# Kernel tuning notes

Hardware: AMD Instinct MI355X
Metric: run time of the kernel (lower is better)

The kernel has to match this reference:

```python
import jax, jax.numpy as jnp
import numpy as np

SEQ, D = 4096, 1024  # vector_size == dimension == 1024


def setup_inputs() -> dict:
    key = jax.random.key(0)
    ks = jax.random.split(key, 7)
    s = 1.0 / np.sqrt(D)
    return {
        "X": jax.random.normal(ks[0], (SEQ, D), dtype=jnp.float32),
        "Wq": jax.random.normal(ks[1], (D, D), dtype=jnp.float32) * s,
        "bq": jax.random.normal(ks[2], (D,), dtype=jnp.float32) * s,
        "Wk": jax.random.normal(ks[3], (D, D), dtype=jnp.float32) * s,
        "bk": jax.random.normal(ks[4], (D,), dtype=jnp.float32) * s,
        "Wv": jax.random.normal(ks[5], (D, D), dtype=jnp.float32) * s,
        "bv": jax.random.normal(ks[6], (D,), dtype=jnp.float32) * s,
    }


def reference(X, Wq, bq, Wk, bk, Wv, bv):
    # Batched QKV projections (nn.Linear: x @ W^T + b), replacing the per-vector loop.
    Q = X @ Wq.T + bq            # [S, D]
    K = X @ Wk.T + bk            # [S, D]
    V = X @ Wv.T + bv            # [S, D]
    scale = 1.0 / jnp.sqrt(jnp.asarray(D, dtype=X.dtype))
    scores = (Q @ K.T) * scale   # [S, S]
    attn = jax.nn.softmax(scores, axis=1)
    return attn @ V              # [S, D]
```

## Files before the change

kernel.cpp:

```cpp
#include <hip/hip_runtime.h>
#include <hip/hip_bf16.h>
#include <stdint.h>


typedef __bf16 bf16_t;
typedef __bf16 bf16x4 __attribute__((ext_vector_type(4)));
typedef __bf16 bf16x8 __attribute__((ext_vector_type(8)));
typedef float f32x4 __attribute__((ext_vector_type(4)));

#define AS1 __attribute__((address_space(1)))
#define AS3 __attribute__((address_space(3)))

__device__ __forceinline__ void async_ld16(const void* g, void* l) {
  __builtin_amdgcn_global_load_lds((AS1 void*)g, (AS3 void*)l, 16, 0, 0);
}

#define SBAR() __builtin_amdgcn_sched_barrier(0)
#define BARRIER()                 \
  do {                            \
    SBAR();                       \
    __builtin_amdgcn_s_barrier(); \
    SBAR();                       \
  } while (0)
#define LGKM0()                                         \
  do {                                                  \
    asm volatile("s_waitcnt lgkmcnt(0)" ::: "memory");  \
    SBAR();                                             \
  } while (0)

template <int MODE>
__global__ __launch_bounds__(512, 2) void gemm8(
    const bf16_t* __restrict__ A, const bf16_t* __restrict__ B, const int ld,
    const int Klen, bf16_t* __restrict__ o0, bf16_t* __restrict__ o1,
    bf16_t* __restrict__ o2, const float* __restrict__ b0,
    const float* __restrict__ b1, const float* __restrict__ b2,
    float* __restrict__ fout, float* __restrict__ rowsum) {
  extern __shared__ bf16_t smem[];

  const int t = threadIdx.x;
  const int lane = t & 63;
  const int wave = t >> 6;
  const int wm = wave >> 2;
  const int wn = wave & 3;
  const int q = lane >> 4;
  const int l16 = lane & 15;
  const int xf = l16 & 7;

  int m0, n0, k0 = 0, zz = 0;
  const int bid = blockIdx.x;
  if constexpr (MODE == 0) {
    const int x = bid & 7, sl = bid >> 3;
    m0 = ((x >> 1) * 4 + (sl & 3)) * 256;
    n0 = ((x & 1) * 6 + (sl >> 2)) * 256;
  } else if constexpr (MODE == 1) {
    const int x = bid & 7, sl = bid >> 3;
    m0 = ((x >> 2) * 8 + (sl >> 2)) * 256;
    n0 = ((x & 3) * 4 + (sl & 3)) * 256;
  } else {
    const int x = bid & 7, sl = bid >> 3;
    zz = x >> 1;
    m0 = ((x & 1) * 8 + (sl >> 2)) * 256;
    n0 = (sl & 3) * 256;
    k0 = zz * Klen;
  }

  const int srow = t >> 3;
  const int c8s = ((t & 7) ^ (srow & 7)) * 8;
  const bf16_t* Ab = A + (size_t)(m0 + srow) * ld + k0 + c8s;
  const bf16_t* Bb = B + (size_t)(n0 + srow) * ld + k0 + c8s;
  const int tl8 = t * 8;

  const int aoff = (wm * 128 + l16) * 64;
  const int boff = (wn * 64 + l16) * 64;
  const int c0 = (q ^ xf) * 8;
  const int c1 = ((4 + q) ^ xf) * 8;

  f32x4 acc[8][4];
  const f32x4 zero4 = {0.f, 0.f, 0.f, 0.f};
#pragma unroll
  for (int i = 0; i < 8; ++i)
#pragma unroll
    for (int j = 0; j < 4; ++j) acc[i][j] = zero4;

  const int NT = Klen >> 6;
  bf16_t* buf0 = smem;
  bf16_t* buf1 = smem + 32768;

  async_ld16(Ab, buf0 + tl8);
  async_ld16(Ab + (size_t)128 * ld, buf0 + 128 * 64 + tl8);
  async_ld16(Bb, buf0 + 16384 + tl8);
  async_ld16(Bb + (size_t)64 * ld, buf0 + 16384 + 64 * 64 + tl8);
  async_ld16(Bb + (size_t)128 * ld, buf0 + 16384 + 128 * 64 + tl8);
  async_ld16(Bb + (size_t)192 * ld, buf0 + 16384 + 192 * 64 + tl8);
  async_ld16(Ab + (size_t)64 * ld, buf0 + 64 * 64 + tl8);
  async_ld16(Ab + (size_t)192 * ld, buf0 + 192 * 64 + tl8);
  async_ld16(Ab + 64, buf1 + tl8);
  async_ld16(Ab + (size_t)128 * ld + 64, buf1 + 128 * 64 + tl8);
  async_ld16(Bb + 64, buf1 + 16384 + tl8);
  async_ld16(Bb + (size_t)64 * ld + 64, buf1 + 16384 + 64 * 64 + tl8);
  async_ld16(Bb + (size_t)128 * ld + 64, buf1 + 16384 + 128 * 64 + tl8);
  async_ld16(Bb + (size_t)192 * ld + 64, buf1 + 16384 + 192 * 64 + tl8);
  asm volatile("s_waitcnt vmcnt(6)" ::: "memory");
  BARRIER();

  for (int T = 0; T < NT; ++T) {
    bf16_t* Ac = (T & 1) ? buf1 : buf0;
    bf16_t* An = (T & 1) ? buf0 : buf1;
    bf16_t* Bc = Ac + 16384;
    const int k1 = (T + 1) << 6;
    const int k2 = (T + 2) << 6;
    const bool s1 = (T + 1) < NT;
    const bool s2 = (T + 2) < NT;

    bf16x8 raA[4][2], raB[4][2], rb[4][2];

#pragma unroll
    for (int im = 0; im < 4; ++im) {
      raA[im][0] = *(const bf16x8*)(Ac + aoff + im * 1024 + c0);
      raA[im][1] = *(const bf16x8*)(Ac + aoff + im * 1024 + c1);
    }
#pragma unroll
    for (int j = 0; j < 4; ++j)
      rb[j][0] = *(const bf16x8*)(Bc + boff + j * 1024 + c0);
    if (s1) {
      async_ld16(Ab + (size_t)64 * ld + k1, An + 64 * 64 + tl8);
      async_ld16(Ab + (size_t)192 * ld + k1, An + 192 * 64 + tl8);
    }
    BARRIER();
    LGKM0();
    __builtin_amdgcn_s_setprio(1);
#pragma unroll
    for (int im = 0; im < 4; ++im)
#pragma unroll
      for (int j = 0; j < 4; ++j)
        acc[im][j] = __builtin_amdgcn_mfma_f32_16x16x32_bf16(
            raA[im][0], rb[j][0], acc[im][j], 0, 0, 0);
    __builtin_amdgcn_s_setprio(0);
    BARRIER();

#pragma unroll
    for (int im = 0; im < 4; ++im)
      raB[im][0] = *(const bf16x8*)(Ac + aoff + (im + 4) * 1024 + c0);
#pragma unroll
    for (int j = 0; j < 4; ++j)
      rb[j][1] = *(const bf16x8*)(Bc + boff + j * 1024 + c1);
    if (s2) {
      async_ld16(Ab + k2, Ac + tl8);
      async_ld16(Ab + (size_t)128 * ld + k2, Ac + 128 * 64 + tl8);
    }
    BARRIER();
    LGKM0();
    __builtin_amdgcn_s_setprio(1);
#pragma unroll
    for (int im = 0; im < 4; ++im)
#pragma unroll
      for (int j = 0; j < 4; ++j)
        acc[4 + im][j] = __builtin_amdgcn_mfma_f32_16x16x32_bf16(
            raB[im][0], rb[j][0], acc[4 + im][j], 0, 0, 0);
    __builtin_amdgcn_s_setprio(0);
    BARRIER();

#pragma unroll
    for (int im = 0; im < 4; ++im)
      raB[im][1] = *(const bf16x8*)(Ac + aoff + (im + 4) * 1024 + c1);
    if (s2) {
      async_ld16(Bb + k2, Bc + tl8);
      async_ld16(Bb + (size_t)64 * ld + k2, Bc + 64 * 64 + tl8);
    }
    BARRIER();
    LGKM0();
    __builtin_amdgcn_s_setprio(1);
#pragma unroll
    for (int im = 0; im < 4; ++im)
#pragma unroll
      for (int j = 0; j < 4; ++j)
        acc[im][j] = __builtin_amdgcn_mfma_f32_16x16x32_bf16(
            raA[im][1], rb[j][1], acc[im][j], 0, 0, 0);
    __builtin_amdgcn_s_setprio(0);
    BARRIER();

    if (s2) {
      async_ld16(Bb + (size_t)128 * ld + k2, Bc + 128 * 64 + tl8);
      async_ld16(Bb + (size_t)192 * ld + k2, Bc + 192 * 64 + tl8);
    }
    BARRIER();
    LGKM0();
    __builtin_amdgcn_s_setprio(1);
#pragma unroll
    for (int im = 0; im < 4; ++im)
#pragma unroll
      for (int j = 0; j < 4; ++j)
        acc[4 + im][j] = __builtin_amdgcn_mfma_f32_16x16x32_bf16(
            raB[im][1], rb[j][1], acc[4 + im][j], 0, 0, 0);
    __builtin_amdgcn_s_setprio(0);
    if (s2) {
      asm volatile("s_waitcnt vmcnt(6)" ::: "memory");
    } else {
      asm volatile("s_waitcnt vmcnt(0)" ::: "memory");
    }
    BARRIER();
  }

  const int mW = m0 + wm * 128 + q * 4;

  if constexpr (MODE == 0) {
    const int sel = n0 >> 10;
    const int nl0 = (n0 & 1023) + wn * 64 + l16;
    if (sel < 2) {
      const float* bias = (sel == 0) ? b0 : b1;
      const float sc = (sel == 0) ? 0.03125f : 1.0f;
      bf16_t* dst = (sel == 0) ? o0 : o1;
#pragma unroll
      for (int j = 0; j < 4; ++j) {
        const int nl = nl0 + j * 16;
        const float bb = bias[nl];
#pragma unroll
        for (int im = 0; im < 8; ++im) {
          const int mr = mW + im * 16;
#pragma unroll
          for (int r = 0; r < 4; ++r)
            dst[(size_t)(mr + r) * 1024 + nl] =
                (bf16_t)((acc[im][j][r] + bb) * sc);
        }
      }
    } else {
      bf16_t* vs = smem;
      const int dg0 = n0 & 1023;
#pragma unroll
      for (int h = 0; h < 2; ++h) {
        if ((wn >> 1) == h) {
#pragma unroll
          for (int j = 0; j < 4; ++j) {
            const int dl = (wn & 1) * 64 + j * 16 + l16;
            const float bb = b2[dg0 + h * 128 + dl];
#pragma unroll
            for (int im = 0; im < 8; ++im) {
              bf16x4 v;
#pragma unroll
              for (int r = 0; r < 4; ++r) v[r] = (bf16_t)(acc[im][j][r] + bb);
              *(bf16x4*)(vs + dl * 264 + wm * 128 + im * 16 + q * 4) = v;
            }
          }
        }
        __syncthreads();
#pragma unroll
        for (int rr = 0; rr < 8; ++rr) {
          const int task = rr * 512 + t;
          const int row = task >> 5, ck = task & 31;
          *(bf16x8*)(o2 + (size_t)(dg0 + h * 128 + row) * 4096 + m0 + ck * 8) =
              *(const bf16x8*)(vs + row * 264 + ck * 8);
        }
        __syncthreads();
      }
    }
  } else if constexpr (MODE == 1) {
    float ps[8][4];
#pragma unroll
    for (int im = 0; im < 8; ++im)
#pragma unroll
      for (int r = 0; r < 4; ++r) ps[im][r] = 0.f;
#pragma unroll
    for (int j = 0; j < 4; ++j) {
      const int n = n0 + wn * 64 + j * 16 + l16;
#pragma unroll
      for (int im = 0; im < 8; ++im) {
        const int mr = mW + im * 16;
#pragma unroll
        for (int r = 0; r < 4; ++r) {
          const float e = __expf(acc[im][j][r]);
          ps[im][r] += e;
          o0[(size_t)(mr + r) * 4096 + n] = (bf16_t)e;
        }
      }
    }
#pragma unroll
    for (int im = 0; im < 8; ++im)
#pragma unroll
      for (int r = 0; r < 4; ++r) {
        float v = ps[im][r];
        v += __shfl_xor(v, 1);
        v += __shfl_xor(v, 2);
        v += __shfl_xor(v, 4);
        v += __shfl_xor(v, 8);
        ps[im][r] = v;
      }
    if (l16 == 0) {
#pragma unroll
      for (int im = 0; im < 8; ++im)
#pragma unroll
        for (int r = 0; r < 4; ++r)
          atomicAdd(rowsum + mW + im * 16 + r, ps[im][r]);
    }
  } else {
    float inv[8][4];
#pragma unroll
    for (int im = 0; im < 8; ++im)
#pragma unroll
      for (int r = 0; r < 4; ++r)
        inv[im][r] = 1.0f / rowsum[mW + im * 16 + r];
    if (zz < 3) {
      bf16_t* pp = (zz == 0) ? o0 : ((zz == 1) ? o1 : o2);
#pragma unroll
      for (int im = 0; im < 8; ++im) {
        const int mr = mW + im * 16;
#pragma unroll
        for (int j = 0; j < 4; ++j) {
          const int n = n0 + wn * 64 + j * 16 + l16;
#pragma unroll
          for (int r = 0; r < 4; ++r)
            pp[(size_t)(mr + r) * 1024 + n] =
                (bf16_t)(acc[im][j][r] * inv[im][r]);
        }
      }
    } else {
#pragma unroll
      for (int im = 0; im < 8; ++im) {
        const int mr = mW + im * 16;
#pragma unroll
        for (int j = 0; j < 4; ++j) {
          const int n = n0 + wn * 64 + j * 16 + l16;
#pragma unroll
          for (int r = 0; r < 4; ++r)
            fout[(size_t)(mr + r) * 1024 + n] = acc[im][j][r] * inv[im][r];
        }
      }
    }
  }
}

__global__ __launch_bounds__(256) void cvt_all(
    const float* __restrict__ X, const float* __restrict__ Wq,
    const float* __restrict__ Wk, const float* __restrict__ Wv,
    bf16_t* __restrict__ Xb, bf16_t* __restrict__ Wb,
    float* __restrict__ rowsum) {
  int i = blockIdx.x * 256 + threadIdx.x;
  if (i >= 1835008) {
    rowsum[i - 1835008] = 0.f;
    return;
  }
  const float* src;
  bf16_t* dst;
  int off;
  if (i < 1048576) {
    src = X; dst = Xb; off = i;
  } else {
    const int w = i - 1048576;
    const int sel = w >> 18;
    off = w & 0x3FFFF;
    src = (sel == 0) ? Wq : ((sel == 1) ? Wk : Wv);
    dst = Wb + (size_t)sel * (1024 * 1024);
  }
  const float4 v = ((const float4*)src)[off];
  bf16x4 o;
  o[0] = (bf16_t)v.x; o[1] = (bf16_t)v.y; o[2] = (bf16_t)v.z; o[3] = (bf16_t)v.w;
  ((bf16x4*)dst)[off] = o;
}

__global__ __launch_bounds__(256) void reduce_out(
    const bf16_t* __restrict__ p0, const bf16_t* __restrict__ p1,
    const bf16_t* __restrict__ p2, float* __restrict__ out) {
  const int i = blockIdx.x * 256 + threadIdx.x;
  const bf16x8 a = ((const bf16x8*)p0)[i];
  const bf16x8 b = ((const bf16x8*)p1)[i];
  const bf16x8 c = ((const bf16x8*)p2)[i];
  float4 lo = ((const float4*)out)[2 * i];
  float4 hi = ((const float4*)out)[2 * i + 1];
  lo.x += (float)a[0] + (float)b[0] + (float)c[0];
  lo.y += (float)a[1] + (float)b[1] + (float)c[1];
  lo.z += (float)a[2] + (float)b[2] + (float)c[2];
  lo.w += (float)a[3] + (float)b[3] + (float)c[3];
  hi.x += (float)a[4] + (float)b[4] + (float)c[4];
  hi.y += (float)a[5] + (float)b[5] + (float)c[5];
  hi.z += (float)a[6] + (float)b[6] + (float)c[6];
  hi.w += (float)a[7] + (float)b[7] + (float)c[7];
  ((float4*)out)[2 * i] = lo;
  ((float4*)out)[2 * i + 1] = hi;
}

extern "C" void kernel_launch(void* const* d_in, const int* in_sizes, int n_in,
                              void* d_out, int out_size, void* d_ws,
                              size_t ws_size, hipStream_t stream) {
  const int S = 4096, D = 1024;
  const float* X  = (const float*)d_in[0];
  const float* Wq = (const float*)d_in[1];
  const float* bq = (const float*)d_in[2];
  const float* Wk = (const float*)d_in[3];
  const float* bk = (const float*)d_in[4];
  const float* Wv = (const float*)d_in[5];
  const float* bv = (const float*)d_in[6];
  float* out = (float*)d_out;

  bf16_t* Xb = (bf16_t*)d_ws;
  bf16_t* Wb = Xb + (size_t)S * D;
  bf16_t* Qb = Wb + (size_t)3 * D * D;
  bf16_t* Kb = Qb + (size_t)S * D;
  bf16_t* Vt = Kb + (size_t)S * D;
  bf16_t* Sc = Vt + (size_t)D * S;
  float* rowsum = (float*)(Sc + (size_t)S * S);

  static int attr_set = 0;
  if (!attr_set) {
    attr_set = 1;
    (void)hipFuncSetAttribute(reinterpret_cast<const void*>(gemm8<0>),
                              hipFuncAttributeMaxDynamicSharedMemorySize,
                              131072);
    (void)hipFuncSetAttribute(reinterpret_cast<const void*>(gemm8<1>),
                              hipFuncAttributeMaxDynamicSharedMemorySize,
                              131072);
    (void)hipFuncSetAttribute(reinterpret_cast<const void*>(gemm8<2>),
                              hipFuncAttributeMaxDynamicSharedMemorySize,
                              131072);
  }

  cvt_all<<<7184, 256, 0, stream>>>(X, Wq, Wk, Wv, Xb, Wb, rowsum);

  gemm8<0><<<192, 512, 131072, stream>>>(
      Xb, Wb, D, D, Qb, Kb, Vt, bq, bk, bv, nullptr, nullptr);
  gemm8<1><<<256, 512, 131072, stream>>>(
      Qb, Kb, D, D, Sc, nullptr, nullptr, nullptr, nullptr, nullptr, nullptr,
      rowsum);
  gemm8<2><<<256, 512, 131072, stream>>>(
      Sc, Vt, S, S / 4, Xb, Qb, Kb, nullptr, nullptr, nullptr, out, rowsum);
  reduce_out<<<S * D / 8 / 256, 256, 0, stream>>>(Xb, Qb, Kb, out);
}
```

Before: 218.2 us.

## Reorder GEMM main-loop phases and drop sched barriers around s_barrier

Restructures the four-phase inner loop so the first two MFMA phases cover A rows 0-127 over both K halves before moving to rows 128-255. It also regroups the async global-to-LDS prefetches (B rows 0-127 now issue earlier, alongside A), and reorders the epilogue store loops to iterate rows outermost with hoisted bias/inverse values. The sched_barrier fences around s_barrier and the lgkm wait are removed, giving the compiler freedom to move LDS reads and MFMAs across barriers. This may improve register live ranges and overlap, but risks the compiler reordering LDS reads relative to async loads and barriers.

```diff
diff --git a/kernel.cpp b/kernel.cpp
--- a/kernel.cpp
+++ b/kernel.cpp
@@ -15,18 +15,8 @@
   __builtin_amdgcn_global_load_lds((AS1 void*)g, (AS3 void*)l, 16, 0, 0);
 }
 
-#define SBAR() __builtin_amdgcn_sched_barrier(0)
-#define BARRIER()                 \
-  do {                            \
-    SBAR();                       \
-    __builtin_amdgcn_s_barrier(); \
-    SBAR();                       \
-  } while (0)
-#define LGKM0()                                         \
-  do {                                                  \
-    asm volatile("s_waitcnt lgkmcnt(0)" ::: "memory");  \
-    SBAR();                                             \
-  } while (0)
+#define BAR() __builtin_amdgcn_s_barrier()
+#define LGKM0() asm volatile("s_waitcnt lgkmcnt(0)" ::: "memory")
 
 template <int MODE>
 __global__ __launch_bounds__(512, 2) void gemm8(
@@ -87,21 +77,21 @@
   bf16_t* buf1 = smem + 32768;
 
   async_ld16(Ab, buf0 + tl8);
-  async_ld16(Ab + (size_t)128 * ld, buf0 + 128 * 64 + tl8);
+  async_ld16(Ab + (size_t)64 * ld, buf0 + 4096 + tl8);
+  async_ld16(Ab + (size_t)128 * ld, buf0 + 8192 + tl8);
+  async_ld16(Ab + (size_t)192 * ld, buf0 + 12288 + tl8);
   async_ld16(Bb, buf0 + 16384 + tl8);
-  async_ld16(Bb + (size_t)64 * ld, buf0 + 16384 + 64 * 64 + tl8);
-  async_ld16(Bb + (size_t)128 * ld, buf0 + 16384 + 128 * 64 + tl8);
-  async_ld16(Bb + (size_t)192 * ld, buf0 + 16384 + 192 * 64 + tl8);
-  async_ld16(Ab + (size_t)64 * ld, buf0 + 64 * 64 + tl8);
-  async_ld16(Ab + (size_t)192 * ld, buf0 + 192 * 64 + tl8);
+  async_ld16(Bb + (size_t)64 * ld, buf0 + 16384 + 4096 + tl8);
+  async_ld16(Bb + (size_t)128 * ld, buf0 + 16384 + 8192 + tl8);
+  async_ld16(Bb + (size_t)192 * ld, buf0 + 16384 + 12288 + tl8);
   async_ld16(Ab + 64, buf1 + tl8);
-  async_ld16(Ab + (size_t)128 * ld + 64, buf1 + 128 * 64 + tl8);
+  async_ld16(Ab + (size_t)128 * ld + 64, buf1 + 8192 + tl8);
   async_ld16(Bb + 64, buf1 + 16384 + tl8);
-  async_ld16(Bb + (size_t)64 * ld + 64, buf1 + 16384 + 64 * 64 + tl8);
-  async_ld16(Bb + (size_t)128 * ld + 64, buf1 + 16384 + 128 * 64 + tl8);
-  async_ld16(Bb + (size_t)192 * ld + 64, buf1 + 16384 + 192 * 64 + tl8);
+  async_ld16(Bb + (size_t)64 * ld + 64, buf1 + 16384 + 4096 + tl8);
+  async_ld16(Bb + (size_t)128 * ld + 64, buf1 + 16384 + 8192 + tl8);
+  async_ld16(Bb + (size_t)192 * ld + 64, buf1 + 16384 + 12288 + tl8);
   asm volatile("s_waitcnt vmcnt(6)" ::: "memory");
-  BARRIER();
+  BAR();
 
   for (int T = 0; T < NT; ++T) {
     bf16_t* Ac = (T & 1) ? buf1 : buf0;
@@ -112,21 +102,19 @@
     const bool s1 = (T + 1) < NT;
     const bool s2 = (T + 2) < NT;
 
-    bf16x8 raA[4][2], raB[4][2], rb[4][2];
-
-#pragma unroll
-    for (int im = 0; im < 4; ++im) {
-      raA[im][0] = *(const bf16x8*)(Ac + aoff + im * 1024 + c0);
-      raA[im][1] = *(const bf16x8*)(Ac + aoff + im * 1024 + c1);
-    }
+    bf16x8 ra0[4], ra1[4], rc0[4], rc1[4], rb0[4], rb1[4];
+
+#pragma unroll
+    for (int im = 0; im < 4; ++im)
+      ra0[im] = *(const bf16x8*)(Ac + aoff + im * 1024 + c0);
 #pragma unroll
     for (int j = 0; j < 4; ++j)
-      rb[j][0] = *(const bf16x8*)(Bc + boff + j * 1024 + c0);
+      rb0[j] = *(const bf16x8*)(Bc + boff + j * 1024 + c0);
     if (s1) {
-      async_ld16(Ab + (size_t)64 * ld + k1, An + 64 * 64 + tl8);
-      async_ld16(Ab + (size_t)192 * ld + k1, An + 192 * 64 + tl8);
-    }
-    BARRIER();
+      async_ld16(Ab + (size_t)64 * ld + k1, An + 4096 + tl8);
+      async_ld16(Ab + (size_t)192 * ld + k1, An + 12288 + tl8);
+    }
+    BAR();
     LGKM0();
     __builtin_amdgcn_s_setprio(1);
 #pragma unroll
@@ -134,21 +122,38 @@
 #pragma unroll
       for (int j = 0; j < 4; ++j)
         acc[im][j] = __builtin_amdgcn_mfma_f32_16x16x32_bf16(
-            raA[im][0], rb[j][0], acc[im][j], 0, 0, 0);
+            ra0[im], rb0[j], acc[im][j], 0, 0, 0);
     __builtin_amdgcn_s_setprio(0);
-    BARRIER();
-
-#pragma unroll
-    for (int im = 0; im < 4; ++im)
-      raB[im][0] = *(const bf16x8*)(Ac + aoff + (im + 4) * 1024 + c0);
+    BAR();
+
+#pragma unroll
+    for (int im = 0; im < 4; ++im)
+      ra1[im] = *(const bf16x8*)(Ac + aoff + im * 1024 + c1);
 #pragma unroll
     for (int j = 0; j < 4; ++j)
-      rb[j][1] = *(const bf16x8*)(Bc + boff + j * 1024 + c1);
+      rb1[j] = *(const bf16x8*)(Bc + boff + j * 1024 + c1);
+    BAR();
+    LGKM0();
+    __builtin_amdgcn_s_setprio(1);
+#pragma unroll
+    for (int im = 0; im < 4; ++im)
+#pragma unroll
+      for (int j = 0; j < 4; ++j)
+        acc[im][j] = __builtin_amdgcn_mfma_f32_16x16x32_bf16(
+            ra1[im], rb1[j], acc[im][j], 0, 0, 0);
+    __builtin_amdgcn_s_setprio(0);
+    BAR();
+
+#pragma unroll
+    for (int im = 0; im < 4; ++im)
+      rc0[im] = *(const bf16x8*)(Ac + aoff + (im + 4) * 1024 + c0);
     if (s2) {
       async_ld16(Ab + k2, Ac + tl8);
-      async_ld16(Ab + (size_t)128 * ld + k2, Ac + 128 * 64 + tl8);
-    }
-    BARRIER();
+      async_ld16(Ab + (size_t)128 * ld + k2, Ac + 8192 + tl8);
+      async_ld16(Bb + k2, Bc + tl8);
+      async_ld16(Bb + (size_t)64 * ld + k2, Bc + 4096 + tl8);
+    }
+    BAR();
     LGKM0();
     __builtin_amdgcn_s_setprio(1);
 #pragma unroll
@@ -156,49 +161,33 @@
 #pragma unroll
       for (int j = 0; j < 4; ++j)
         acc[4 + im][j] = __builtin_amdgcn_mfma_f32_16x16x32_bf16(
-            raB[im][0], rb[j][0], acc[4 + im][j], 0, 0, 0);
+            rc0[im], rb0[j], acc[4 + im][j], 0, 0, 0);
     __builtin_amdgcn_s_setprio(0);
-    BARRIER();
-
-#pragma unroll
-    for (int im = 0; im < 4; ++im)
-      raB[im][1] = *(const bf16x8*)(Ac + aoff + (im + 4) * 1024 + c1);
+    BAR();
+
+#pragma unroll
+    for (int im = 0; im < 4; ++im)
+      rc1[im] = *(const bf16x8*)(Ac + aoff + (im + 4) * 1024 + c1);
     if (s2) {
-      async_ld16(Bb + k2, Bc + tl8);
-      async_ld16(Bb + (size_t)64 * ld + k2, Bc + 64 * 64 + tl8);
-    }
-    BARRIER();
+      async_ld16(Bb + (size_t)128 * ld + k2, Bc + 8192 + tl8);
+      async_ld16(Bb + (size_t)192 * ld + k2, Bc + 12288 + tl8);
+    }
+    BAR();
     LGKM0();
     __builtin_amdgcn_s_setprio(1);
 #pragma unroll
     for (int im = 0; im < 4; ++im)
 #pragma unroll
       for (int j = 0; j < 4; ++j)
-        acc[im][j] = __builtin_amdgcn_mfma_f32_16x16x32_bf16(
-            raA[im][1], rb[j][1], acc[im][j], 0, 0, 0);
-    __builtin_amdgcn_s_setprio(0);
-    BARRIER();
-
-    if (s2) {
-      async_ld16(Bb + (size_t)128 * ld + k2, Bc + 128 * 64 + tl8);
-      async_ld16(Bb + (size_t)192 * ld + k2, Bc + 192 * 64 + tl8);
-    }
-    BARRIER();
-    LGKM0();
-    __builtin_amdgcn_s_setprio(1);
-#pragma unroll
-    for (int im = 0; im < 4; ++im)
-#pragma unroll
-      for (int j = 0; j < 4; ++j)
         acc[4 + im][j] = __builtin_amdgcn_mfma_f32_16x16x32_bf16(
-            raB[im][1], rb[j][1], acc[4 + im][j], 0, 0, 0);
+            rc1[im], rb1[j], acc[4 + im][j], 0, 0, 0);
     __builtin_amdgcn_s_setprio(0);
     if (s2) {
       asm volatile("s_waitcnt vmcnt(6)" ::: "memory");
     } else {
       asm volatile("s_waitcnt vmcnt(0)" ::: "memory");
     }
-    BARRIER();
+    BAR();
   }
 
   const int mW = m0 + wm * 128 + q * 4;
@@ -210,18 +199,18 @@
       const float* bias = (sel == 0) ? b0 : b1;
       const float sc = (sel == 0) ? 0.03125f : 1.0f;
       bf16_t* dst = (sel == 0) ? o0 : o1;
-#pragma unroll
-      for (int j = 0; j < 4; ++j) {
-        const int nl = nl0 + j * 16;
-        const float bb = bias[nl];
-#pragma unroll
-        for (int im = 0; im < 8; ++im) {
-          const int mr = mW + im * 16;
-#pragma unroll
-          for (int r = 0; r < 4; ++r)
-            dst[(size_t)(mr + r) * 1024 + nl] =
-                (bf16_t)((acc[im][j][r] + bb) * sc);
-        }
+      float bb[4];
+#pragma unroll
+      for (int j = 0; j < 4; ++j) bb[j] = bias[nl0 + j * 16];
+#pragma unroll
+      for (int im = 0; im < 8; ++im) {
+        const int mr = mW + im * 16;
+#pragma unroll
+        for (int r = 0; r < 4; ++r)
+#pragma unroll
+          for (int j = 0; j < 4; ++j)
+            dst[(size_t)(mr + r) * 1024 + nl0 + j * 16] =
+                (bf16_t)((acc[im][j][r] + bb[j]) * sc);
       }
     } else {
       bf16_t* vs = smem;
@@ -259,19 +248,18 @@
     for (int im = 0; im < 8; ++im)
 #pragma unroll
       for (int r = 0; r < 4; ++r) ps[im][r] = 0.f;
-#pragma unroll
-    for (int j = 0; j < 4; ++j) {
-      const int n = n0 + wn * 64 + j * 16 + l16;
-#pragma unroll
-      for (int im = 0; im < 8; ++im) {
-        const int mr = mW + im * 16;
-#pragma unroll
-        for (int r = 0; r < 4; ++r) {
+    const int nb = n0 + wn * 64 + l16;
+#pragma unroll
+    for (int im = 0; im < 8; ++im) {
+      const int mr = mW + im * 16;
+#pragma unroll
+      for (int r = 0; r < 4; ++r)
+#pragma unroll
+        for (int j = 0; j < 4; ++j) {
           const float e = __expf(acc[im][j][r]);
           ps[im][r] += e;
-          o0[(size_t)(mr + r) * 4096 + n] = (bf16_t)e;
+          o0[(size_t)(mr + r) * 4096 + nb + j * 16] = (bf16_t)e;
         }
-      }
     }
 #pragma unroll
     for (int im = 0; im < 8; ++im)
@@ -298,18 +286,19 @@
 #pragma unroll
       for (int r = 0; r < 4; ++r)
         inv[im][r] = 1.0f / rowsum[mW + im * 16 + r];
+    const int nb = n0 + wn * 64 + l16;
     if (zz < 3) {
       bf16_t* pp = (zz == 0) ? o0 : ((zz == 1) ? o1 : o2);
 #pragma unroll
       for (int im = 0; im < 8; ++im) {
         const int mr = mW + im * 16;
 #pragma unroll
-        for (int j = 0; j < 4; ++j) {
-          const int n = n0 + wn * 64 + j * 16 + l16;
-#pragma unroll
-          for (int r = 0; r < 4; ++r)
-            pp[(size_t)(mr + r) * 1024 + n] =
-                (bf16_t)(acc[im][j][r] * inv[im][r]);
+        for (int r = 0; r < 4; ++r) {
+          const float iv = inv[im][r];
+#pragma unroll
+          for (int j = 0; j < 4; ++j)
+            pp[(size_t)(mr + r) * 1024 + nb + j * 16] =
+                (bf16_t)(acc[im][j][r] * iv);
         }
       }
     } else {
@@ -317,11 +306,11 @@
       for (int im = 0; im < 8; ++im) {
         const int mr = mW + im * 16;
 #pragma unroll
-        for (int j = 0; j < 4; ++j) {
-          const int n = n0 + wn * 64 + j * 16 + l16;
-#pragma unroll
-          for (int r = 0; r < 4; ++r)
-            fout[(size_t)(mr + r) * 1024 + n] = acc[im][j][r] * inv[im][r];
+        for (int r = 0; r < 4; ++r) {
+          const float iv = inv[im][r];
+#pragma unroll
+          for (int j = 0; j < 4; ++j)
+            fout[(size_t)(mr + r) * 1024 + nb + j * 16] = acc[im][j][r] * iv;
         }
       }
     }
```

Result: no change. 215.7 us (-1.1%).
